# Kernel tuning notes

Measured on AMD Instinct MI355X. Metric: run time of the kernel, lower is better.

Reference implementation:

```python
import jax, jax.numpy as jnp
import numpy as np

B, N, E, H, A = 64, 64, 4032, 256, 4  # batch, max atoms, edges per mol, hidden, edge-attr dim
FI = 2 * H + 1 + A  # edge-MLP input dim = 517
SCALE = 15.0


def setup_inputs() -> dict:
    key = jax.random.key(0)
    ks = jax.random.split(key, 16)
    w = lambda k, s: jax.random.normal(k, s, jnp.float32) * 0.05
    # edge indices with i != j to avoid degenerate zero-distance edges
    ii = jax.random.randint(ks[3], (B, E), 0, N)
    off = jax.random.randint(ks[4], (B, E), 1, N)
    jj = (ii + off) % N
    edge_indices = jnp.stack([ii, jj], axis=-1).astype(jnp.int32)
    return dict(
        x=jax.random.normal(ks[0], (B, N, 3), jnp.float32),
        h=jax.random.normal(ks[1], (B, N, H), jnp.float32),
        a=jax.random.normal(ks[2], (B, E, A), jnp.float32),
        edge_indices=edge_indices,
        node_mask=jnp.ones((B, N, 1), jnp.float32),
        edge_mask=jnp.ones((B, E, 1), jnp.float32),
        We1=w(ks[5], (FI, 256)), be1=jnp.zeros(256, jnp.float32),
        We2=w(ks[6], (256, 256)), be2=jnp.zeros(256, jnp.float32),
        Wa=w(ks[7], (256, 1)), ba=jnp.zeros(1, jnp.float32),
        Wh1=w(ks[8], (H + 256, 256)), bh1=jnp.zeros(256, jnp.float32),
        Wh2=w(ks[9], (256, 256)), bh2=jnp.zeros(256, jnp.float32),
        Wx1=w(ks[10], (FI, 256)), bx1=jnp.zeros(256, jnp.float32),
        Wx2=w(ks[11], (256, 256)), bx2=jnp.zeros(256, jnp.float32),
        Wx3=w(ks[12], (256, 1)),
    )


def reference(x, h, a, edge_indices, node_mask, edge_mask,
              We1, be1, We2, be2, Wa, ba,
              Wh1, bh1, Wh2, bh2, Wx1, bx1, Wx2, bx2, Wx3):
    silu = jax.nn.silu
    bidx = jnp.arange(B)[:, None]                      # [B,1] batch gather index
    ii, jj = edge_indices[..., 0], edge_indices[..., 1]
    x_i, x_j = x[bidx, ii], x[bidx, jj]                # [B,E,3]
    diff = (x_i - x_j) * edge_mask                     # [B,E,3]
    d = jnp.sqrt(jnp.sum(diff * diff, -1, keepdims=True))  # [B,E,1]
    h_i, h_j = h[bidx, ii], h[bidx, jj]                # [B,E,H]
    feat = jnp.concatenate([h_i, h_j, d * d, a], -1)   # [B,E,517]
    # edge MLP + attention gate
    m = silu(silu(feat @ We1 + be1) @ We2 + be2)       # [B,E,256]
    e = jax.nn.sigmoid(m @ Wa + ba)                    # [B,E,1]
    em = e * m
    # scatter-add to source nodes (replaces the one-hot matmul, same math)
    seg = (bidx * N + ii).reshape(-1)                  # [B*E]
    em_agg = jax.ops.segment_sum(em.reshape(B * E, 256), seg,
                                 num_segments=B * N).reshape(B, N, 256)
    h_out = (h + silu(jnp.concatenate([h, em_agg], -1) @ Wh1 + bh1) @ Wh2 + bh2) * node_mask
    # coordinate update
    xw = jnp.tanh(silu(silu(feat @ Wx1 + bx1) @ Wx2 + bx2) @ Wx3) * SCALE  # [B,E,1]
    xm = xw * diff / (d + 1.0)                         # [B,E,3]
    x_agg = jax.ops.segment_sum(xm.reshape(B * E, 3), seg,
                                num_segments=B * N).reshape(B, N, 3)
    x_out = (x + x_agg) * node_mask
    return x_out, h_out
```

## Files before the change

### kernel.cpp

```cpp
#include <hip/hip_runtime.h>

#define E_ 4032
#define TE 64
#define NB 4032

typedef unsigned int uint;
typedef unsigned short ushort;
typedef __attribute__((ext_vector_type(8))) short short8;
typedef __attribute__((ext_vector_type(4))) float f32x4;
typedef __attribute__((ext_vector_type(2))) float f32x2;

__device__ __forceinline__ ushort f2bf(float x) {
  uint u = __float_as_uint(x);
  return (ushort)((u + 0x7fffu + ((u >> 16) & 1u)) >> 16);
}
__device__ __forceinline__ uint cvtpk(float lo, float hi) {
  uint r;
  asm("v_cvt_pk_bf16_f32 %0, %1, %2" : "=v"(r) : "v"(lo), "v"(hi));
  return r;
}
__device__ __forceinline__ float exp2_(float x) {
  float r;
  asm("v_exp_f32 %0, %1" : "=v"(r) : "v"(x));
  return r;
}
__device__ __forceinline__ float bflo(uint u) { return __uint_as_float(u << 16); }
__device__ __forceinline__ float bfhi(uint u) { return __uint_as_float(u & 0xffff0000u); }
__device__ __forceinline__ float bf2f(ushort s) { return __uint_as_float((uint)s << 16); }
__device__ __forceinline__ float rcp_(float x) { return __builtin_amdgcn_rcpf(x); }
__device__ __forceinline__ float silu_(float v) { return v * rcp_(1.0f + exp2_(v * -1.44269504f)); }
__device__ __forceinline__ float sigmoid_(float v) { return rcp_(1.0f + exp2_(v * -1.44269504f)); }
__device__ __forceinline__ float tanh_(float v) { return 1.0f - 2.0f * rcp_(1.0f + exp2_(v * 2.88539008f)); }

__device__ __forceinline__ f32x2 silu2(f32x2 v) {
  f32x2 nm = v * (f32x2){-1.44269504f, -1.44269504f};
  f32x2 e = {exp2_(nm.x), exp2_(nm.y)};
  f32x2 den = e + (f32x2){1.0f, 1.0f};
  f32x2 r = {rcp_(den.x), rcp_(den.y)};
  return v * r;
}

__device__ __forceinline__ void atom_pk_bf16(ushort* p, uint v) {
  asm volatile("global_atomic_pk_add_bf16 %0, %1, off" :: "v"(p), "v"(v) : "memory");
}

template <int RM>
__device__ __forceinline__ void gemmT(const ushort* Ab, const ushort* Bmat,
                                      int w, int l15, int lhi, f32x4 acc[RM][4]) {
#pragma unroll
  for (int ks = 0; ks < 8; ++ks) {
    short8 bv[4];
#pragma unroll
    for (int cn = 0; cn < 4; ++cn) {
      int col = w * 64 + cn * 16 + l15;
      bv[cn] = *(const short8*)(Bmat + col * 256 + ks * 32 + lhi * 8);
    }
    short8 av[RM];
#pragma unroll
    for (int rm = 0; rm < RM; ++rm) {
      int row = rm * 16 + l15;
      int byt = (ks * 64 + lhi * 16) ^ ((row & 7) << 4);
      av[rm] = *(const short8*)((const char*)Ab + row * 512 + byt);
    }
#pragma unroll
    for (int cn = 0; cn < 4; ++cn)
#pragma unroll
      for (int rm = 0; rm < RM; ++rm)
        acc[rm][cn] = __builtin_amdgcn_mfma_f32_16x16x32_bf16(av[rm], bv[cn], acc[rm][cn], 0, 0, 0);
  }
}

__global__ __launch_bounds__(256) void k_count_prep(
    const int* __restrict__ eidx, uint* __restrict__ cnt,
    const float* __restrict__ We1, const float* __restrict__ Wx1,
    const float* __restrict__ Wh1, const float* __restrict__ We2,
    const float* __restrict__ Wx2, const float* __restrict__ Wh2,
    ushort* __restrict__ WT, uint4* __restrict__ zbase) {
  __shared__ float tl[64][65];
  int bid = blockIdx.x;
  int t = threadIdx.x;
  if (bid < 1008) {
    int g = bid * 256 + t;
    int b = g / E_;
    int i = eidx[(size_t)g * 2];
    atomicAdd(&cnt[b * 64 + i], 1u);
    return;
  }
  if (bid >= 1152) {
    uint4* z = zbase + (size_t)((bid - 1152) * 256 + t) * 4;
    uint4 zz = {0u, 0u, 0u, 0u};
    z[0] = zz; z[1] = zz; z[2] = zz; z[3] = zz;
    return;
  }
  int blk = bid - 1008;
  int m = blk >> 4, tile = blk & 15;
  int kt = (tile & 3) * 64, nt = (tile >> 2) * 64;
  const float* src;
  switch (m) {
    case 0: src = We1; break;
    case 1: src = We1 + 65536; break;
    case 2: src = Wx1; break;
    case 3: src = Wx1 + 65536; break;
    case 4: src = Wh1; break;
    case 5: src = We2; break;
    case 6: src = Wx2; break;
    case 7: src = Wh1 + 65536; break;
    default: src = Wh2; break;
  }
  int c = t & 63, r4 = t >> 6;
#pragma unroll
  for (int rr = 0; rr < 64; rr += 4)
    tl[rr + r4][c] = src[(size_t)(kt + rr + r4) * 256 + nt + c];
  __syncthreads();
#pragma unroll
  for (int rr = 0; rr < 64; rr += 4)
    WT[(size_t)m * 65536 + (size_t)(nt + rr + r4) * 256 + kt + c] = f2bf(tl[c][rr + r4]);
}

__global__ __launch_bounds__(256) void k_scan(const uint* __restrict__ cnt,
                                              uint* __restrict__ cursor) {
  __shared__ uint sw[4];
  int t = threadIdx.x;
  uint loc[16];
  uint tot = 0;
#pragma unroll
  for (int q = 0; q < 16; ++q) {
    loc[q] = cnt[t * 16 + q];
    tot += loc[q];
  }
  uint v = tot;
#pragma unroll
  for (int d = 1; d < 64; d <<= 1) {
    uint u = __shfl_up(v, d);
    if ((t & 63) >= d) v += u;
  }
  if ((t & 63) == 63) sw[t >> 6] = v;
  __syncthreads();
  uint woff = 0;
  int wv = t >> 6;
  if (wv > 0) woff += sw[0];
  if (wv > 1) woff += sw[1];
  if (wv > 2) woff += sw[2];
  uint run = woff + v - tot;
#pragma unroll
  for (int q = 0; q < 16; ++q) {
    cursor[t * 16 + q] = run;
    run += loc[q];
  }
}

__global__ __launch_bounds__(256, 2) void k_fill_proj(
    const int* __restrict__ eidx, uint* __restrict__ cursor,
    uint* __restrict__ perm, const float* __restrict__ h,
    const ushort* __restrict__ WT, ushort* __restrict__ P) {
  __shared__ ushort Ab[128 * 256];
  int bid = blockIdx.x;
  int t = threadIdx.x;
  if (bid < 1008) {
    int g = bid * 256 + t;
    int b = g / E_;
    int i = eidx[(size_t)g * 2];
    uint slot = atomicAdd(&cursor[b * 64 + i], 1u);
    perm[slot] = (uint)g;
    return;
  }
  int blk = bid - 1008;
  int rowbase = (blk & 31) * 128;
  int g = blk >> 5;
  {
    int c2 = t & 127, es = t >> 7;
#pragma unroll 4
    for (int it = 0; it < 64; ++it) {
      int row = it * 2 + es;
      float2 v = *(const float2*)(h + (size_t)(rowbase + row) * 256 + c2 * 2);
      *(uint*)((char*)Ab + row * 512 + ((c2 * 4) ^ ((row & 7) << 4))) = cvtpk(v.x, v.y);
    }
  }
  __syncthreads();
  int w = t >> 6, lane = t & 63, l15 = lane & 15, lhi = lane >> 4;
  f32x4 acc[8][4] = {};
  gemmT<8>(Ab, WT + g * 65536, w, l15, lhi, acc);
#pragma unroll
  for (int rm = 0; rm < 8; ++rm)
#pragma unroll
    for (int cn = 0; cn < 4; ++cn)
#pragma unroll
      for (int r = 0; r < 4; ++r) {
        int row = rowbase + rm * 16 + lhi * 4 + r;
        int col = w * 64 + cn * 16 + l15;
        P[(size_t)row * 1280 + g * 256 + col] = f2bf(acc[rm][cn][r]);
      }
}

__device__ __forceinline__ void buildT1(int t, const uint* __restrict__ Pu,
                                        const float* __restrict__ Wbig,
                                        const float* __restrict__ b1, int offI,
                                        ushort* Ab, const uint* s_pio,
                                        const uint* s_pjo,
                                        const float* s_d2, const float4* s_a4) {
  int c2 = t & 63, es = t >> 6;
  int c0 = c2 * 4;
  const float* Wr = Wbig + 512 * 256 + c0;
  f32x2 w5A = *(const f32x2*)(Wr);        f32x2 w5B = *(const f32x2*)(Wr + 2);
  f32x2 a0A = *(const f32x2*)(Wr + 256);  f32x2 a0B = *(const f32x2*)(Wr + 258);
  f32x2 a1A = *(const f32x2*)(Wr + 512);  f32x2 a1B = *(const f32x2*)(Wr + 514);
  f32x2 a2A = *(const f32x2*)(Wr + 768);  f32x2 a2B = *(const f32x2*)(Wr + 770);
  f32x2 a3A = *(const f32x2*)(Wr + 1024); f32x2 a3B = *(const f32x2*)(Wr + 1026);
  f32x2 bbA = *(const f32x2*)(b1 + c0);   f32x2 bbB = *(const f32x2*)(b1 + c0 + 2);
  const uint* Pme = Pu + (uint)(offI + c2 * 2);
  const uint* Pmj = Pu + (uint)(offI + 128 + c2 * 2);
#pragma unroll 2
  for (int it = 0; it < 16; ++it) {
    int e = it * 4 + es;
    uint2 pi = *(const uint2*)(Pme + s_pio[e]);
    uint2 pj = *(const uint2*)(Pmj + s_pjo[e]);
    f32x2 d2v;
    d2v.x = s_d2[e];
    d2v.y = d2v.x;
    float4 av = s_a4[e];
    f32x2 vA = (f32x2){bflo(pi.x), bfhi(pi.x)} + (f32x2){bflo(pj.x), bfhi(pj.x)};
    f32x2 vB = (f32x2){bflo(pi.y), bfhi(pi.y)} + (f32x2){bflo(pj.y), bfhi(pj.y)};
    f32x2 axv = {av.x, av.x}, ayv = {av.y, av.y}, azv = {av.z, av.z}, awv = {av.w, av.w};
    f32x2 zA = bbA + d2v * w5A + axv * a0A + ayv * a1A + azv * a2A + awv * a3A;
    f32x2 zB = bbB + d2v * w5B + axv * a0B + ayv * a1B + azv * a2B + awv * a3B;
    vA = silu2(vA + zA);
    vB = silu2(vB + zB);
    uint2 o;
    o.x = cvtpk(vA.x, vA.y);
    o.y = cvtpk(vB.x, vB.y);
    *(uint2*)((char*)Ab + e * 512 + ((c0 * 2) ^ ((e & 7) << 4))) = o;
  }
}

__global__ __launch_bounds__(256, 4) void k_edge(
    const float* __restrict__ x, const int* __restrict__ eidx,
    const float* __restrict__ a, const float* __restrict__ emask,
    const uint* __restrict__ perm,
    const ushort* __restrict__ P, const ushort* __restrict__ WT,
    const float* __restrict__ We1, const float* __restrict__ be1,
    const float* __restrict__ be2, const float* __restrict__ Wa,
    const float* __restrict__ ba,
    const float* __restrict__ Wx1, const float* __restrict__ bx1,
    const float* __restrict__ bx2, const float* __restrict__ Wx3,
    ushort* __restrict__ em_agg, float* __restrict__ x_agg) {
  __shared__ ushort Ab[TE * 256];
  __shared__ uint s_ij[TE];
  __shared__ uint s_pio[TE], s_pjo[TE];
  __shared__ float s_d2[TE];
  __shared__ float4 s_a4[TE];
  __shared__ float s_dx[TE], s_dy[TE], s_dz[TE];
  __shared__ float s_red[2][TE];
  __shared__ ushort s_seghead[TE + 2];
  __shared__ int s_nseg;
  int t = threadIdx.x;
  int bid = blockIdx.x;
  bid = (bid & 7) * 504 + (bid >> 3);
  int ebase = bid * TE;

  if (t < TE) {
    int eid = (int)perm[ebase + t];
    int b = ebase / E_;
    int2 ij = *(const int2*)(eidx + (size_t)eid * 2);
    uint i4 = (uint)(b * 64 + ij.x);
    uint j4 = (uint)(b * 64 + ij.y);
    s_ij[t] = i4 | (j4 << 16);
    s_pio[t] = i4 * 640u;
    s_pjo[t] = j4 * 640u;
    float m = emask[eid];
    float dx = (x[i4 * 3 + 0] - x[j4 * 3 + 0]) * m;
    float dy = (x[i4 * 3 + 1] - x[j4 * 3 + 1]) * m;
    float dz = (x[i4 * 3 + 2] - x[j4 * 3 + 2]) * m;
    s_d2[t] = dx * dx + dy * dy + dz * dz;
    s_dx[t] = dx; s_dy[t] = dy; s_dz[t] = dz;
    s_a4[t] = *(const float4*)(a + (size_t)eid * 4);
    s_red[0][t] = 0.f;
    s_red[1][t] = 0.f;
    uint prev = __shfl_up(i4, 1);
    int flag = (t == 0) || (i4 != prev);
    unsigned long long mask = __ballot(flag);
    int rank = (int)__popcll(mask & ((1ull << t) - 1ull));
    if (flag) s_seghead[rank] = (ushort)t;
    if (t == 0) {
      int ns = (int)__popcll(mask);
      s_nseg = ns;
      s_seghead[ns] = TE;
    }
  }
  __syncthreads();

  const uint* Pu = (const uint*)P;
  int w = t >> 6, lane = t & 63, l15 = lane & 15, lhi = lane >> 4;
  float ba0 = ba[0];

  buildT1(t, Pu, Wx1, bx1, 256, Ab, s_pio, s_pjo, s_d2, s_a4);
  __syncthreads();
  {
    f32x4 acc1[4][4] = {};
    __builtin_amdgcn_s_setprio(1);
    gemmT<4>(Ab, WT + 6 * 65536, w, l15, lhi, acc1);
    __builtin_amdgcn_s_setprio(0);
    int colb = w * 64 + l15;
    f32x2 wvA = {Wx3[colb], Wx3[colb + 16]};
    f32x2 wvB = {Wx3[colb + 32], Wx3[colb + 48]};
    f32x2 b2A = {bx2[colb], bx2[colb + 16]};
    f32x2 b2B = {bx2[colb + 32], bx2[colb + 48]};
#pragma unroll
    for (int rm = 0; rm < 4; ++rm)
#pragma unroll
      for (int r = 0; r < 4; ++r) {
        f32x2 mA = silu2((f32x2){acc1[rm][0][r], acc1[rm][1][r]} + b2A);
        f32x2 mB = silu2((f32x2){acc1[rm][2][r], acc1[rm][3][r]} + b2B);
        f32x2 q = mA * wvA + mB * wvB;
        float p = q.x + q.y;
        p += __shfl_xor(p, 1);
        p += __shfl_xor(p, 2);
        p += __shfl_xor(p, 4);
        p += __shfl_xor(p, 8);
        if (l15 == 0) atomicAdd(&s_red[1][rm * 16 + lhi * 4 + r], p);
      }
  }
  __syncthreads();

  buildT1(t, Pu, We1, be1, 0, Ab, s_pio, s_pjo, s_d2, s_a4);
  __syncthreads();

  {
    int ns = s_nseg;
    for (int s = w; s < ns; s += 4) {
      int st = s_seghead[s], en = s_seghead[s + 1];
      int r = st + lane;
      float sx = 0.f, sy = 0.f, sz = 0.f;
      if (r < en) {
        float fac = tanh_(s_red[1][r]) * 15.0f * rcp_(sqrtf(s_d2[r]) + 1.0f);
        sx = fac * s_dx[r]; sy = fac * s_dy[r]; sz = fac * s_dz[r];
      }
#pragma unroll
      for (int d = 1; d < 64; d <<= 1) {
        sx += __shfl_xor(sx, d);
        sy += __shfl_xor(sy, d);
        sz += __shfl_xor(sz, d);
      }
      if (lane == 0) {
        uint i4 = s_ij[st] & 0xffffu;
        atomicAdd(x_agg + i4 * 3u + 0, sx);
        atomicAdd(x_agg + i4 * 3u + 1, sy);
        atomicAdd(x_agg + i4 * 3u + 2, sz);
      }
    }
  }

  f32x4 acc0[4][4] = {};
  __builtin_amdgcn_s_setprio(1);
  gemmT<4>(Ab, WT + 5 * 65536, w, l15, lhi, acc0);
  __builtin_amdgcn_s_setprio(0);
  {
    int colb = w * 64 + l15;
    f32x2 wvA = {Wa[colb], Wa[colb + 16]};
    f32x2 wvB = {Wa[colb + 32], Wa[colb + 48]};
    f32x2 b2A = {be2[colb], be2[colb + 16]};
    f32x2 b2B = {be2[colb + 32], be2[colb + 48]};
#pragma unroll
    for (int rm = 0; rm < 4; ++rm)
#pragma unroll
      for (int r = 0; r < 4; ++r) {
        f32x2 mA = silu2((f32x2){acc0[rm][0][r], acc0[rm][1][r]} + b2A);
        f32x2 mB = silu2((f32x2){acc0[rm][2][r], acc0[rm][3][r]} + b2B);
        acc0[rm][0][r] = mA.x; acc0[rm][1][r] = mA.y;
        acc0[rm][2][r] = mB.x; acc0[rm][3][r] = mB.y;
        f32x2 q = mA * wvA + mB * wvB;
        float p = q.x + q.y;
        p += __shfl_xor(p, 1);
        p += __shfl_xor(p, 2);
        p += __shfl_xor(p, 4);
        p += __shfl_xor(p, 8);
        if (l15 == 0) atomicAdd(&s_red[0][rm * 16 + lhi * 4 + r], p);
      }
  }
  __syncthreads();

  uint* AbU = (uint*)Ab;
#pragma unroll
  for (int rm = 0; rm < 4; ++rm)
#pragma unroll
    for (int r = 0; r < 4; ++r) {
      int row = rm * 16 + lhi * 4 + r;
      float g = sigmoid_(s_red[0][row] + ba0);
#pragma unroll
      for (int cn = 0; cn < 4; ++cn) {
        float vme = g * acc0[rm][cn][r];
        float vpo = __shfl_xor(vme, 1);
        if (!(l15 & 1)) {
          int cp = (w * 64 + cn * 16 + l15) >> 1;
          AbU[row * 128 + cp] = cvtpk(vme, vpo);
        }
      }
    }
  __syncthreads();

  {
    int ns = s_nseg;
    int c = t & 127;
    for (int s = t >> 7; s < ns; s += 2) {
      int st = s_seghead[s], en = s_seghead[s + 1];
      f32x2 sum = {0.f, 0.f};
      for (int r = st; r < en; ++r) {
        uint u = AbU[r * 128 + c];
        sum += (f32x2){bflo(u), bfhi(u)};
      }
      uint i4 = s_ij[st] & 0xffffu;
      atom_pk_bf16(em_agg + i4 * 256u + (uint)(c * 2), cvtpk(sum.x, sum.y));
    }
  }
}

__global__ __launch_bounds__(256, 2) void k_node(
    const float* __restrict__ h, const float* __restrict__ x,
    const float* __restrict__ nmask,
    const ushort* __restrict__ em_agg, const float* __restrict__ x_agg,
    const ushort* __restrict__ P, const ushort* __restrict__ WT,
    const float* __restrict__ bh1, const float* __restrict__ bh2,
    float* __restrict__ out) {
  __shared__ ushort Ab[32 * 256];
  int t = threadIdx.x;
  int rowbase = blockIdx.x * 32;
  {
    const uint* emu = (const uint*)em_agg;
    int c2 = t & 127, es = t >> 7;
#pragma unroll 4
    for (int it = 0; it < 16; ++it) {
      int row = it * 2 + es;
      uint v = emu[(size_t)(rowbase + row) * 128 + c2];
      *(uint*)((char*)Ab + row * 512 + ((c2 * 4) ^ ((row & 7) << 4))) = v;
    }
  }
  __syncthreads();
  int w = t >> 6, lane = t & 63, l15 = lane & 15, lhi = lane >> 4;
  {
    f32x4 acc[2][4] = {};
    gemmT<2>(Ab, WT + 7 * 65536, w, l15, lhi, acc);
    __syncthreads();
    float bc[4];
#pragma unroll
    for (int cn = 0; cn < 4; ++cn) bc[cn] = bh1[w * 64 + cn * 16 + l15];
#pragma unroll
    for (int rm = 0; rm < 2; ++rm)
#pragma unroll
      for (int cn = 0; cn < 4; ++cn)
#pragma unroll
        for (int r = 0; r < 4; ++r) {
          int row = rm * 16 + lhi * 4 + r;
          int col = w * 64 + cn * 16 + l15;
          float q1 = bf2f(P[(size_t)(rowbase + row) * 1280 + 1024 + col]);
          float sv = silu_(acc[rm][cn][r] + q1 + bc[cn]);
          *(ushort*)((char*)Ab + row * 512 + ((col * 2) ^ ((row & 7) << 4))) = f2bf(sv);
        }
  }
  __syncthreads();
  {
    f32x4 acc[2][4] = {};
    gemmT<2>(Ab, WT + 8 * 65536, w, l15, lhi, acc);
    float bc[4];
#pragma unroll
    for (int cn = 0; cn < 4; ++cn) bc[cn] = bh2[w * 64 + cn * 16 + l15];
#pragma unroll
    for (int rm = 0; rm < 2; ++rm)
#pragma unroll
      for (int cn = 0; cn < 4; ++cn)
#pragma unroll
        for (int r = 0; r < 4; ++r) {
          int row = rowbase + rm * 16 + lhi * 4 + r;
          int col = w * 64 + cn * 16 + l15;
          float o = (h[(size_t)row * 256 + col] + acc[rm][cn][r] + bc[cn]) * nmask[row];
          out[12288 + (size_t)row * 256 + col] = o;
        }
  }
  if (t < 32) {
    int row = rowbase + t;
    float nm = nmask[row];
#pragma unroll
    for (int c = 0; c < 3; ++c)
      out[row * 3 + c] = (x[row * 3 + c] + x_agg[row * 3 + c]) * nm;
  }
}

extern "C" void kernel_launch(void* const* d_in, const int* in_sizes, int n_in,
                              void* d_out, int out_size, void* d_ws, size_t ws_size,
                              hipStream_t stream) {
  (void)in_sizes; (void)n_in; (void)out_size; (void)ws_size;
  const float* x = (const float*)d_in[0];
  const float* h = (const float*)d_in[1];
  const float* a = (const float*)d_in[2];
  const int* eidx = (const int*)d_in[3];
  const float* nmask = (const float*)d_in[4];
  const float* emask = (const float*)d_in[5];
  const float* We1 = (const float*)d_in[6];
  const float* be1 = (const float*)d_in[7];
  const float* We2 = (const float*)d_in[8];
  const float* be2 = (const float*)d_in[9];
  const float* Wa = (const float*)d_in[10];
  const float* ba = (const float*)d_in[11];
  const float* Wh1 = (const float*)d_in[12];
  const float* bh1 = (const float*)d_in[13];
  const float* Wh2 = (const float*)d_in[14];
  const float* bh2 = (const float*)d_in[15];
  const float* Wx1 = (const float*)d_in[16];
  const float* bx1 = (const float*)d_in[17];
  const float* Wx2 = (const float*)d_in[18];
  const float* bx2 = (const float*)d_in[19];
  const float* Wx3 = (const float*)d_in[20];

  char* ws = (char*)d_ws;
  ushort* WT = (ushort*)ws;
  ushort* P = (ushort*)(ws + 1179648);
  ushort* em_agg = (ushort*)(ws + 11665408);
  float* x_agg = (float*)(ws + 13762560);
  uint* cnt = (uint*)(ws + 13811712);
  uint* cursor = (uint*)(ws + 13828096);
  uint* perm = (uint*)(ws + 13844480);

  hipMemsetAsync(cnt, 0, 16384, stream);
  k_count_prep<<<1283, 256, 0, stream>>>(eidx, cnt, We1, Wx1, Wh1, We2, Wx2, Wh2,
                                         WT, (uint4*)em_agg);
  k_scan<<<1, 256, 0, stream>>>(cnt, cursor);
  k_fill_proj<<<1168, 256, 0, stream>>>(eidx, cursor, perm, h, WT, P);
  k_edge<<<NB, 256, 0, stream>>>(x, eidx, a, emask, perm, P, WT, We1, be1, be2, Wa, ba,
                                 Wx1, bx1, bx2, Wx3, em_agg, x_agg);
  k_node<<<128, 256, 0, stream>>>(h, x, nmask, em_agg, x_agg, P, WT, bh1, bh2,
                                  (float*)d_out);
}
```

Baseline: 265.3 us.

## Alternate edge-MLP branch order across blocks to desynchronize phases

Factors the GEMM epilogue, em dump, em reduction and x scatter into helpers. Half of the blocks, chosen by blockIdx bit 3, now run the attention branch first and the coordinate branch second, while the other half keep the original order. The aim is to stagger phases between co-resident blocks so MFMA-heavy GEMM phases overlap with the build and atomic phases of other blocks. In the swapped order acc0 stays live across the second GEMM, which raises register pressure and risks spills under launch_bounds(256,4).

After: 341.1 us. +28.6%, slower.

```diff
diff --git a/kernel.cpp b/kernel.cpp
--- a/kernel.cpp
+++ b/kernel.cpp
@@ -232,6 +232,109 @@
   }
 }
 
+template <bool KEEP>
+__device__ __forceinline__ void gemm_epi(const ushort* Ab, const ushort* Bmat,
+                                         const float* __restrict__ wv,
+                                         const float* __restrict__ b2,
+                                         float* __restrict__ red,
+                                         int w, int l15, int lhi, f32x4 acc[4][4]) {
+#pragma unroll
+  for (int rm = 0; rm < 4; ++rm)
+#pragma unroll
+    for (int cn = 0; cn < 4; ++cn) acc[rm][cn] = (f32x4){0.f, 0.f, 0.f, 0.f};
+  __builtin_amdgcn_s_setprio(1);
+  gemmT<4>(Ab, Bmat, w, l15, lhi, acc);
+  __builtin_amdgcn_s_setprio(0);
+  int colb = w * 64 + l15;
+  f32x2 wvA = {wv[colb], wv[colb + 16]};
+  f32x2 wvB = {wv[colb + 32], wv[colb + 48]};
+  f32x2 b2A = {b2[colb], b2[colb + 16]};
+  f32x2 b2B = {b2[colb + 32], b2[colb + 48]};
+#pragma unroll
+  for (int rm = 0; rm < 4; ++rm)
+#pragma unroll
+    for (int r = 0; r < 4; ++r) {
+      f32x2 mA = silu2((f32x2){acc[rm][0][r], acc[rm][1][r]} + b2A);
+      f32x2 mB = silu2((f32x2){acc[rm][2][r], acc[rm][3][r]} + b2B);
+      if (KEEP) {
+        acc[rm][0][r] = mA.x; acc[rm][1][r] = mA.y;
+        acc[rm][2][r] = mB.x; acc[rm][3][r] = mB.y;
+      }
+      f32x2 q = mA * wvA + mB * wvB;
+      float p = q.x + q.y;
+      p += __shfl_xor(p, 1);
+      p += __shfl_xor(p, 2);
+      p += __shfl_xor(p, 4);
+      p += __shfl_xor(p, 8);
+      if (l15 == 0) atomicAdd(&red[rm * 16 + lhi * 4 + r], p);
+    }
+}
+
+__device__ __forceinline__ void dump_em(f32x4 acc0[4][4], const float* __restrict__ red0,
+                                        float ba0, int w, int l15, int lhi, uint* AbU) {
+#pragma unroll
+  for (int rm = 0; rm < 4; ++rm)
+#pragma unroll
+    for (int r = 0; r < 4; ++r) {
+      int row = rm * 16 + lhi * 4 + r;
+      float g = sigmoid_(red0[row] + ba0);
+#pragma unroll
+      for (int cn = 0; cn < 4; ++cn) {
+        float vme = g * acc0[rm][cn][r];
+        float vpo = __shfl_xor(vme, 1);
+        if (!(l15 & 1)) {
+          int cp = (w * 64 + cn * 16 + l15) >> 1;
+          AbU[row * 128 + cp] = cvtpk(vme, vpo);
+        }
+      }
+    }
+}
+
+__device__ __forceinline__ void em_reduce(int t, int ns, const ushort* seghead,
+                                          const uint* s_ij, const uint* AbU,
+                                          ushort* __restrict__ em_agg) {
+  int c = t & 127;
+  for (int s = t >> 7; s < ns; s += 2) {
+    int st = seghead[s], en = seghead[s + 1];
+    f32x2 sum = {0.f, 0.f};
+    for (int r = st; r < en; ++r) {
+      uint u = AbU[r * 128 + c];
+      sum += (f32x2){bflo(u), bfhi(u)};
+    }
+    uint i4 = s_ij[st] & 0xffffu;
+    atom_pk_bf16(em_agg + i4 * 256u + (uint)(c * 2), cvtpk(sum.x, sum.y));
+  }
+}
+
+__device__ __forceinline__ void x_scatter(int w, int lane, int ns,
+                                          const ushort* seghead, const uint* s_ij,
+                                          const float* __restrict__ red1,
+                                          const float* s_d2, const float* s_dx,
+                                          const float* s_dy, const float* s_dz,
+                                          float* __restrict__ x_agg) {
+  for (int s = w; s < ns; s += 4) {
+    int st = seghead[s], en = seghead[s + 1];
+    int r = st + lane;
+    float sx = 0.f, sy = 0.f, sz = 0.f;
+    if (r < en) {
+      float fac = tanh_(red1[r]) * 15.0f * rcp_(sqrtf(s_d2[r]) + 1.0f);
+      sx = fac * s_dx[r]; sy = fac * s_dy[r]; sz = fac * s_dz[r];
+    }
+#pragma unroll
+    for (int d = 1; d < 64; d <<= 1) {
+      sx += __shfl_xor(sx, d);
+      sy += __shfl_xor(sy, d);
+      sz += __shfl_xor(sz, d);
+    }
+    if (lane == 0) {
+      uint i4 = s_ij[st] & 0xffffu;
+      atomicAdd(x_agg + i4 * 3u + 0, sx);
+      atomicAdd(x_agg + i4 * 3u + 1, sy);
+      atomicAdd(x_agg + i4 * 3u + 2, sz);
+    }
+  }
+}
+
 __global__ __launch_bounds__(256, 4) void k_edge(
     const float* __restrict__ x, const int* __restrict__ eidx,
     const float* __restrict__ a, const float* __restrict__ emask,
@@ -254,6 +357,7 @@
   __shared__ int s_nseg;
   int t = threadIdx.x;
   int bid = blockIdx.x;
+  int swap = (bid >> 3) & 1;
   bid = (bid & 7) * 504 + (bid >> 3);
   int ebase = bid * TE;
 
@@ -291,125 +395,41 @@
   const uint* Pu = (const uint*)P;
   int w = t >> 6, lane = t & 63, l15 = lane & 15, lhi = lane >> 4;
   float ba0 = ba[0];
-
-  buildT1(t, Pu, Wx1, bx1, 256, Ab, s_pio, s_pjo, s_d2, s_a4);
-  __syncthreads();
-  {
-    f32x4 acc1[4][4] = {};
-    __builtin_amdgcn_s_setprio(1);
-    gemmT<4>(Ab, WT + 6 * 65536, w, l15, lhi, acc1);
-    __builtin_amdgcn_s_setprio(0);
-    int colb = w * 64 + l15;
-    f32x2 wvA = {Wx3[colb], Wx3[colb + 16]};
-    f32x2 wvB = {Wx3[colb + 32], Wx3[colb + 48]};
-    f32x2 b2A = {bx2[colb], bx2[colb + 16]};
-    f32x2 b2B = {bx2[colb + 32], bx2[colb + 48]};
-#pragma unroll
-    for (int rm = 0; rm < 4; ++rm)
-#pragma unroll
-      for (int r = 0; r < 4; ++r) {
-        f32x2 mA = silu2((f32x2){acc1[rm][0][r], acc1[rm][1][r]} + b2A);
-        f32x2 mB = silu2((f32x2){acc1[rm][2][r], acc1[rm][3][r]} + b2B);
-        f32x2 q = mA * wvA + mB * wvB;
-        float p = q.x + q.y;
-        p += __shfl_xor(p, 1);
-        p += __shfl_xor(p, 2);
-        p += __shfl_xor(p, 4);
-        p += __shfl_xor(p, 8);
-        if (l15 == 0) atomicAdd(&s_red[1][rm * 16 + lhi * 4 + r], p);
-      }
-  }
-  __syncthreads();
-
-  buildT1(t, Pu, We1, be1, 0, Ab, s_pio, s_pjo, s_d2, s_a4);
-  __syncthreads();
-
-  {
-    int ns = s_nseg;
-    for (int s = w; s < ns; s += 4) {
-      int st = s_seghead[s], en = s_seghead[s + 1];
-      int r = st + lane;
-      float sx = 0.f, sy = 0.f, sz = 0.f;
-      if (r < en) {
-        float fac = tanh_(s_red[1][r]) * 15.0f * rcp_(sqrtf(s_d2[r]) + 1.0f);
-        sx = fac * s_dx[r]; sy = fac * s_dy[r]; sz = fac * s_dz[r];
-      }
-#pragma unroll
-      for (int d = 1; d < 64; d <<= 1) {
-        sx += __shfl_xor(sx, d);
-        sy += __shfl_xor(sy, d);
-        sz += __shfl_xor(sz, d);
-      }
-      if (lane == 0) {
-        uint i4 = s_ij[st] & 0xffffu;
-        atomicAdd(x_agg + i4 * 3u + 0, sx);
-        atomicAdd(x_agg + i4 * 3u + 1, sy);
-        atomicAdd(x_agg + i4 * 3u + 2, sz);
-      }
-    }
-  }
-
-  f32x4 acc0[4][4] = {};
-  __builtin_amdgcn_s_setprio(1);
-  gemmT<4>(Ab, WT + 5 * 65536, w, l15, lhi, acc0);
-  __builtin_amdgcn_s_setprio(0);
-  {
-    int colb = w * 64 + l15;
-    f32x2 wvA = {Wa[colb], Wa[colb + 16]};
-    f32x2 wvB = {Wa[colb + 32], Wa[colb + 48]};
-    f32x2 b2A = {be2[colb], be2[colb + 16]};
-    f32x2 b2B = {be2[colb + 32], be2[colb + 48]};
-#pragma unroll
-    for (int rm = 0; rm < 4; ++rm)
-#pragma unroll
-      for (int r = 0; r < 4; ++r) {
-        f32x2 mA = silu2((f32x2){acc0[rm][0][r], acc0[rm][1][r]} + b2A);
-        f32x2 mB = silu2((f32x2){acc0[rm][2][r], acc0[rm][3][r]} + b2B);
-        acc0[rm][0][r] = mA.x; acc0[rm][1][r] = mA.y;
-        acc0[rm][2][r] = mB.x; acc0[rm][3][r] = mB.y;
-        f32x2 q = mA * wvA + mB * wvB;
-        float p = q.x + q.y;
-        p += __shfl_xor(p, 1);
-        p += __shfl_xor(p, 2);
-        p += __shfl_xor(p, 4);
-        p += __shfl_xor(p, 8);
-        if (l15 == 0) atomicAdd(&s_red[0][rm * 16 + lhi * 4 + r], p);
-      }
-  }
-  __syncthreads();
-
   uint* AbU = (uint*)Ab;
-#pragma unroll
-  for (int rm = 0; rm < 4; ++rm)
-#pragma unroll
-    for (int r = 0; r < 4; ++r) {
-      int row = rm * 16 + lhi * 4 + r;
-      float g = sigmoid_(s_red[0][row] + ba0);
-#pragma unroll
-      for (int cn = 0; cn < 4; ++cn) {
-        float vme = g * acc0[rm][cn][r];
-        float vpo = __shfl_xor(vme, 1);
-        if (!(l15 & 1)) {
-          int cp = (w * 64 + cn * 16 + l15) >> 1;
-          AbU[row * 128 + cp] = cvtpk(vme, vpo);
-        }
-      }
-    }
-  __syncthreads();
-
-  {
-    int ns = s_nseg;
-    int c = t & 127;
-    for (int s = t >> 7; s < ns; s += 2) {
-      int st = s_seghead[s], en = s_seghead[s + 1];
-      f32x2 sum = {0.f, 0.f};
-      for (int r = st; r < en; ++r) {
-        uint u = AbU[r * 128 + c];
-        sum += (f32x2){bflo(u), bfhi(u)};
-      }
-      uint i4 = s_ij[st] & 0xffffu;
-      atom_pk_bf16(em_agg + i4 * 256u + (uint)(c * 2), cvtpk(sum.x, sum.y));
-    }
+  f32x4 acc0[4][4];
+
+  if (!swap) {
+    buildT1(t, Pu, Wx1, bx1, 256, Ab, s_pio, s_pjo, s_d2, s_a4);
+    __syncthreads();
+    {
+      f32x4 acc1[4][4];
+      gemm_epi<false>(Ab, WT + 6 * 65536, Wx3, bx2, s_red[1], w, l15, lhi, acc1);
+    }
+    __syncthreads();
+    buildT1(t, Pu, We1, be1, 0, Ab, s_pio, s_pjo, s_d2, s_a4);
+    __syncthreads();
+    x_scatter(w, lane, s_nseg, s_seghead, s_ij, s_red[1], s_d2, s_dx, s_dy, s_dz, x_agg);
+    gemm_epi<true>(Ab, WT + 5 * 65536, Wa, be2, s_red[0], w, l15, lhi, acc0);
+    __syncthreads();
+    dump_em(acc0, s_red[0], ba0, w, l15, lhi, AbU);
+    __syncthreads();
+    em_reduce(t, s_nseg, s_seghead, s_ij, AbU, em_agg);
+  } else {
+    buildT1(t, Pu, We1, be1, 0, Ab, s_pio, s_pjo, s_d2, s_a4);
+    __syncthreads();
+    gemm_epi<true>(Ab, WT + 5 * 65536, Wa, be2, s_red[0], w, l15, lhi, acc0);
+    __syncthreads();
+    buildT1(t, Pu, Wx1, bx1, 256, Ab, s_pio, s_pjo, s_d2, s_a4);
+    __syncthreads();
+    {
+      f32x4 acc1[4][4];
+      gemm_epi<false>(Ab, WT + 6 * 65536, Wx3, bx2, s_red[1], w, l15, lhi, acc1);
+    }
+    __syncthreads();
+    dump_em(acc0, s_red[0], ba0, w, l15, lhi, AbU);
+    __syncthreads();
+    em_reduce(t, s_nseg, s_seghead, s_ij, AbU, em_agg);
+    x_scatter(w, lane, s_nseg, s_seghead, s_ij, s_red[1], s_d2, s_dx, s_dy, s_dz, x_agg);
   }
 }
 
```
